# Performance work log

Measured on AMD Instinct MI355X. Metric: run time of the kernel, lower is better.

Reference implementation:

```python
import jax, jax.numpy as jnp
import numpy as np

WS = 16          # window_size
OWS = 24         # overlap_win_size = int(ws*0.5) + ws
PAD = (OWS - WS) // 2
NH = 6           # num_heads


def _ln(x, g, b):
    m = jnp.mean(x, axis=-1, keepdims=True)
    v = jnp.mean((x - m) ** 2, axis=-1, keepdims=True)
    return (x - m) * jax.lax.rsqrt(v + 1e-5) * g + b


def setup_inputs() -> dict:
    key = jax.random.key(0)
    ks = jax.random.split(key, 12)
    B, H, W, C = 4, 64, 64, 180
    std = 0.02
    x = jax.random.normal(ks[0], (B, H * W, C), jnp.float32)
    y = jax.random.normal(ks[1], (B, H * W, C), jnp.float32)
    kv_w = jax.random.normal(ks[2], (2 * C, C), jnp.float32) * std
    kv_b = jnp.zeros((2 * C,), jnp.float32)
    q_w = jax.random.normal(ks[3], (C, C), jnp.float32) * std
    q_b = jnp.zeros((C,), jnp.float32)
    rpb = jax.random.normal(ks[4], ((WS + OWS - 1) ** 2, NH), jnp.float32) * std
    proj_w = jax.random.normal(ks[5], (C, C), jnp.float32) * std
    proj_b = jnp.zeros((C,), jnp.float32)
    fc1_w = jax.random.normal(ks[6], (4 * C, C), jnp.float32) * std
    fc1_b = jnp.zeros((4 * C,), jnp.float32)
    fc2_w = jax.random.normal(ks[7], (C, 4 * C), jnp.float32) * std
    fc2_b = jnp.zeros((C,), jnp.float32)
    norm1_g = jnp.ones((C,), jnp.float32); norm1_b = jnp.zeros((C,), jnp.float32)
    norm2_g = jnp.ones((C,), jnp.float32); norm2_b = jnp.zeros((C,), jnp.float32)
    # relative position index (HAT-style OCA): query coords vs extended window coords
    co = np.stack(np.meshgrid(np.arange(WS), np.arange(WS), indexing='ij')).reshape(2, -1)   # 2, ws*ws
    ce = np.stack(np.meshgrid(np.arange(OWS), np.arange(OWS), indexing='ij')).reshape(2, -1) # 2, ows*ows
    rel = (ce[:, None, :] - co[:, :, None]).transpose(1, 2, 0) + (WS - 1)  # nq, n, 2 in [0, ws+ows-2]
    rpi = jnp.asarray(rel[..., 0] * (WS + OWS - 1) + rel[..., 1], jnp.int32)  # [256, 576]
    return {
        'x': x, 'y': y,
        'norm1_g': norm1_g, 'norm1_b': norm1_b,
        'kv_w': kv_w, 'kv_b': kv_b, 'q_w': q_w, 'q_b': q_b,
        'rpb': rpb, 'proj_w': proj_w, 'proj_b': proj_b,
        'norm2_g': norm2_g, 'norm2_b': norm2_b,
        'fc1_w': fc1_w, 'fc1_b': fc1_b, 'fc2_w': fc2_w, 'fc2_b': fc2_b,
        'rpi': rpi, 'h': 64, 'w': 64,
    }


def reference(x, y, norm1_g, norm1_b, kv_w, kv_b, q_w, q_b, rpb, proj_w, proj_b,
              norm2_g, norm2_b, fc1_w, fc1_b, fc2_w, fc2_b, rpi, h, w):
    b, L, c = x.shape
    nh = NH
    d = c // nh
    scale = d ** -0.5
    nwh, nww = h // WS, w // WS
    nq, n = WS * WS, OWS * OWS

    shortcut = x
    xn = _ln(x, norm1_g, norm1_b).reshape(b, h, w, c)
    yn = _ln(y, norm1_g, norm1_b).reshape(b, h, w, c)

    kv = xn @ kv_w.T + kv_b                                  # b,h,w,2c
    q = yn @ q_w.T + q_b                                     # b,h,w,c

    # kv -> [2, b, c, h, w] then pad spatially and extract overlapping windows (nn.Unfold)
    kv = kv.reshape(b, h, w, 2, c).transpose(3, 0, 4, 1, 2)  # 2,b,c,h,w
    kvp = jnp.pad(kv, ((0, 0), (0, 0), (0, 0), (PAD, PAD), (PAD, PAD)))
    hh = jnp.arange(nwh)[:, None] * WS + jnp.arange(OWS)[None, :]   # [nwh, OWS]
    ww = jnp.arange(nww)[:, None] * WS + jnp.arange(OWS)[None, :]   # [nww, OWS]
    patches = kvp[:, :, :, hh][:, :, :, :, :, ww]            # 2,b,c,nwh,OWS,nww,OWS
    kvw = patches.transpose(0, 1, 3, 5, 4, 6, 2).reshape(2, b * nwh * nww, n, c)
    kwin, vwin = kvw[0], kvw[1]                              # [b_, n, c]

    # non-overlapping query windows (window_partition)
    qwin = q.reshape(b, nwh, WS, nww, WS, c).transpose(0, 1, 3, 2, 4, 5).reshape(-1, nq, c)
    b_ = qwin.shape[0]

    qh = qwin.reshape(b_, nq, nh, d).transpose(0, 2, 1, 3) * scale
    kh = kwin.reshape(b_, n, nh, d).transpose(0, 2, 1, 3)
    vh = vwin.reshape(b_, n, nh, d).transpose(0, 2, 1, 3)

    attn = jnp.einsum('bhqd,bhkd->bhqk', qh, kh)             # [b_, nh, nq, n]
    bias = rpb[rpi.reshape(-1)].reshape(nq, n, nh).transpose(2, 0, 1)  # [nh, nq, n]
    attn = jax.nn.softmax(attn + bias[None], axis=-1)
    out = jnp.einsum('bhqk,bhkd->bhqd', attn, vh).transpose(0, 2, 1, 3).reshape(b_, nq, c)

    # window_reverse
    out = out.reshape(b, nwh, nww, WS, WS, c).transpose(0, 1, 3, 2, 4, 5).reshape(b, h * w, c)

    xo = out @ proj_w.T + proj_b + shortcut
    xn2 = _ln(xo, norm2_g, norm2_b)
    mlp = jax.nn.gelu(xn2 @ fc1_w.T + fc1_b, approximate=False) @ fc2_w.T + fc2_b
    return xo + mlp
```

## Files before the change

### kernel.cpp

```cpp
#include <hip/hip_runtime.h>

typedef __bf16 bf16;
typedef __bf16 bf16x8 __attribute__((ext_vector_type(8)));
typedef __bf16 bf16x4 __attribute__((ext_vector_type(4)));
typedef __bf16 bf16x2 __attribute__((ext_vector_type(2)));
typedef float f32x4 __attribute__((ext_vector_type(4)));

static __device__ __forceinline__ bf16x8 ld8(const bf16* p) {
    return *reinterpret_cast<const bf16x8*>(p);
}
static __device__ __forceinline__ bf16x4 ld4(const bf16* p) {
    return *reinterpret_cast<const bf16x4*>(p);
}
static __device__ __forceinline__ bf16x8 ld8_b32(const bf16* p) {
    bf16x8 v;
#pragma unroll
    for (int i = 0; i < 4; ++i) {
        bf16x2 t = *reinterpret_cast<const bf16x2*>(p + i * 2);
        v[i * 2] = t[0]; v[i * 2 + 1] = t[1];
    }
    return v;
}
static __device__ __forceinline__ bf16x8 zero8() {
    bf16x8 v;
#pragma unroll
    for (int i = 0; i < 8; ++i) v[i] = (bf16)0.f;
    return v;
}

#define MFMA16(a, b, c) __builtin_amdgcn_mfma_f32_16x16x32_bf16((a), (b), (c), 0, 0, 0)

template <int ROWS, int BK, int KPAD, int THREADS>
static __device__ __forceinline__ void load_chunk_g(const bf16* __restrict__ g,
                                                    bf16x8* r, int tid) {
    constexpr int TOT = ROWS * BK / 8;
    constexpr int NP = (TOT + THREADS - 1) / THREADS;
#pragma unroll
    for (int p = 0; p < NP; ++p) {
        int idx = p * THREADS + tid;
        if ((TOT % THREADS) == 0 || idx < TOT) {
            int row = idx / (BK / 8), cg = idx % (BK / 8);
            r[p] = ld8(g + (long)row * KPAD + cg * 8);
        }
    }
}
template <int ROWS, int BK, int THREADS>
static __device__ __forceinline__ void store_chunk_l(bf16* __restrict__ lds,
                                                     const bf16x8* r, int tid) {
    constexpr int TOT = ROWS * BK / 8;
    constexpr int NP = (TOT + THREADS - 1) / THREADS;
#pragma unroll
    for (int p = 0; p < NP; ++p) {
        int idx = p * THREADS + tid;
        if ((TOT % THREADS) == 0 || idx < TOT) {
            int row = idx / (BK / 8), cg = idx % (BK / 8);
            *reinterpret_cast<bf16x8*>(lds + row * 200 + cg * 8) = r[p];
        }
    }
}
template <int ROWS, int BK, int KPAD, int THREADS>
static __device__ __forceinline__ void stage_tile(const bf16* __restrict__ g,
                                                  bf16* __restrict__ lds, int tid) {
    constexpr int TOT = ROWS * BK / 8;
    constexpr int NP = (TOT + THREADS - 1) / THREADS;
#pragma unroll
    for (int p = 0; p < NP; ++p) {
        int idx = p * THREADS + tid;
        if ((TOT % THREADS) == 0 || idx < TOT) {
            int row = idx / (BK / 8), cg = idx % (BK / 8);
            bf16x8 v = ld8(g + (long)row * KPAD + cg * 8);
            *reinterpret_cast<bf16x8*>(lds + row * 200 + cg * 8) = v;
        }
    }
}

__global__ __launch_bounds__(256) void fused_pre(
    const float* __restrict__ x, const float* __restrict__ y,
    const float* __restrict__ g, const float* __restrict__ b,
    bf16* __restrict__ dst,
    const float* __restrict__ kv_w, const float* __restrict__ kv_b,
    const float* __restrict__ q_w, const float* __restrict__ q_b,
    const float* __restrict__ proj_w, const float* __restrict__ fc1_w,
    const float* __restrict__ fc2_w, const float* __restrict__ rpb,
    const int* __restrict__ rpi,
    bf16* __restrict__ wkv, bf16* __restrict__ wq, bf16* __restrict__ wproj,
    bf16* __restrict__ wfc1, bf16* __restrict__ wfc2, bf16* __restrict__ biast,
    float* __restrict__ kvbp, float* __restrict__ qbp)
{
    for (int u = blockIdx.x; u < 13635; u += 1704) {
        if (u < 8192) {
            int wave = threadIdx.x >> 6, lane = threadIdx.x & 63;
            int row = u * 4 + wave;
            const float* sp = (row < 16384) ? (x + (long)row * 180)
                                            : (y + (long)(row - 16384) * 180);
            float v0 = sp[lane];
            float v1 = sp[lane + 64];
            float v2 = (lane < 52) ? sp[lane + 128] : 0.f;
            float s = v0 + v1 + v2;
            float sq = v0 * v0 + v1 * v1 + v2 * v2;
#pragma unroll
            for (int m = 32; m >= 1; m >>= 1) {
                s += __shfl_xor(s, m);
                sq += __shfl_xor(sq, m);
            }
            float mean = s * (1.f / 180.f);
            float var = sq * (1.f / 180.f) - mean * mean;
            float rs = rsqrtf(var + 1e-5f);
            bf16* dp = dst + (long)row * 192;
            dp[lane] = (bf16)((v0 - mean) * rs * g[lane] + b[lane]);
            dp[lane + 64] = (bf16)((v1 - mean) * rs * g[lane + 64] + b[lane + 64]);
            float o2 = (lane < 52) ? ((v2 - mean) * rs * g[lane + 128] + b[lane + 128]) : 0.f;
            dp[lane + 128] = (bf16)o2;
            continue;
        }
        int i = (u - 8192) * 256 + threadIdx.x;
        if (i < 73728) {
            int n = i / 192, k = i % 192;
            int kv = n / 192, rem = n % 192, hh = rem >> 5, d = rem & 31;
            float v = (d < 30 && k < 180) ? kv_w[(kv * 180 + hh * 30 + d) * 180 + k] : 0.f;
            wkv[i] = (bf16)v;
        } else if (i < 122880) {
            int j = i - 73728; int n = j / 192, k = j % 192;
            int hh = n >> 5, d = n & 31;
            float v = (n < 192 && d < 30 && k < 180) ? q_w[(hh * 30 + d) * 180 + k] : 0.f;
            wq[j] = (bf16)v;
        } else if (i < 172032) {
            int j = i - 122880; int n = j / 192, k = j % 192;
            int hh = k >> 5, d = k & 31;
            float v = (n < 180 && d < 30) ? proj_w[n * 180 + hh * 30 + d] : 0.f;
            wproj[j] = (bf16)v;
        } else if (i < 319488) {
            int j = i - 172032; int n = j / 192, k = j % 192;
            float v = (n < 720 && k < 180) ? fc1_w[n * 180 + k] : 0.f;
            wfc1[j] = (bf16)v;
        } else if (i < 507904) {
            int j = i - 319488; int n = j / 736, k = j % 736;
            float v = (n < 180 && k < 720) ? fc2_w[n * 720 + k] : 0.f;
            wfc2[j] = (bf16)v;
        } else if (i < 1392640) {
            int t = i - 507904;
            int r = t & 3;
            int lane = (t >> 2) & 63;
            int tmp2 = t >> 8;
            int kg = tmp2 % 36;
            int tmp3 = tmp2 / 36;
            int qg = tmp3 & 15;
            int h = tmp3 >> 4;
            int q = qg * 16 + (lane & 15);
            int key = kg * 16 + ((lane >> 4) << 2) + r;
            biast[t] = (bf16)rpb[rpi[q * 576 + key] * 6 + h];
        } else if (i < 1393024) {
            int t = i - 1392640;
            int kv = t / 192, rem = t % 192, hh = rem >> 5, d = rem & 31;
            kvbp[t] = (d < 30) ? kv_b[kv * 180 + hh * 30 + d] : 0.f;
        } else if (i < 1393216) {
            int t = i - 1393024;
            int hh = t >> 5, d = t & 31;
            qbp[t] = (d < 30) ? q_b[hh * 30 + d] * 0.18257418583505537f : 0.f;
        }
    }
}

__global__ __launch_bounds__(512, 4) void gemm_kvq(
    const bf16* __restrict__ xn, const bf16* __restrict__ yn,
    const bf16* __restrict__ wkv, const bf16* __restrict__ wq,
    const float* __restrict__ kvbp, const float* __restrict__ qbp,
    bf16* __restrict__ kvbuf, bf16* __restrict__ qbuf)
{
    const int tid = threadIdx.x, wave = tid >> 6, lane = tid & 63;
    const int llo = lane & 15, quad = lane >> 4;
    const int phys = blockIdx.x;
    const int xcd = phys & 7, idx = phys >> 3;
    const int tmi = xcd * 16 + idx / 3;
    const int bz = idx % 3;
    const bool isq = (bz == 2);
    const bf16* A = isq ? yn : xn;
    const bf16* Wbase = isq ? wq : (wkv + (long)bz * 3 * 64 * 192);
    const int tm = tmi * 128;

    __shared__ __align__(16) bf16 Sa[128 * 200];
    __shared__ __align__(16) bf16 Sb[64 * 200];
    bf16* Sc = Sb;

    stage_tile<128, 192, 192, 512>(A + (long)tm * 192, Sa, tid);
    bf16x8 wreg[3];
    load_chunk_g<64, 192, 192, 512>(Wbase, wreg, tid);

    const float sc = isq ? 0.18257418583505537f : 1.f;

    for (int s = 0; s < 3; ++s) {
        if (s) __syncthreads();
        store_chunk_l<64, 192, 512>(Sb, wreg, tid);
        __syncthreads();
        if (s < 2) load_chunk_g<64, 192, 192, 512>(Wbase + (long)(s + 1) * 64 * 192, wreg, tid);

        f32x4 acc[4];
#pragma unroll
        for (int nt = 0; nt < 4; ++nt)
#pragma unroll
            for (int r = 0; r < 4; ++r) acc[nt][r] = 0.f;
#pragma unroll
        for (int kt = 0; kt < 6; ++kt) {
            bf16x8 a = ld8(Sa + (wave * 16 + llo) * 200 + kt * 32 + quad * 8);
#pragma unroll
            for (int nt = 0; nt < 4; ++nt) {
                bf16x8 b = ld8(Sb + (nt * 16 + llo) * 200 + kt * 32 + quad * 8);
                acc[nt] = MFMA16(a, b, acc[nt]);
            }
        }

        const int grp = bz * 3 + s;
        __syncthreads();
#pragma unroll
        for (int nt = 0; nt < 4; ++nt) {
            int n = grp * 64 + nt * 16 + llo;
            float bv = isq ? qbp[n - 384] : kvbp[n];
#pragma unroll
            for (int r = 0; r < 4; ++r)
                Sc[(wave * 16 + quad * 4 + r) * 72 + nt * 16 + llo] =
                    (bf16)(acc[nt][r] * sc + bv);
        }
        __syncthreads();
        const int row8 = tid >> 3, seg = tid & 7;
#pragma unroll
        for (int ps = 0; ps < 2; ++ps) {
            int row = ps * 64 + row8;
            bf16x8 vv = *reinterpret_cast<const bf16x8*>(Sc + row * 72 + seg * 8);
            long m = tm + row;
            if (!isq)
                *reinterpret_cast<bf16x8*>(kvbuf + m * 384 + grp * 64 + seg * 8) = vv;
            else
                *reinterpret_cast<bf16x8*>(qbuf + m * 192 + (grp - 6) * 64 + seg * 8) = vv;
        }
    }
}

__global__ __launch_bounds__(512, 6) void attn_kernel(
    const bf16* __restrict__ qbuf, const bf16* __restrict__ kvbuf,
    const bf16* __restrict__ biast, bf16* __restrict__ obuf)
{
    const int phys = blockIdx.x;
    const int xcd = phys & 7, idx = phys >> 3;
    const int win = xcd * 8 + idx / 12;
    const int sub = idx % 12;
    const int qhalf = sub & 1;
    const int head = sub >> 1;
    const int bb = win / 16, wi = (win % 16) / 4, wj = win % 4;
    const int tid = threadIdx.x;
    const int wave = tid >> 6, lane = tid & 63;
    const int llo = lane & 15, quad = lane >> 4;
    const int qbase = qhalf * 128 + wave * 16;
    const int qg = qhalf * 8 + wave;

    __shared__ bf16 Kc[2][64][40];
    __shared__ bf16 Vt[2][32][74];
    __shared__ bf16 Ps[8][16][72];

    const int u = tid & 255;
    const int tloc = u >> 2, dq = u & 3;
    const bool isV = tid >= 256;
    int aa = tloc / 24, w0 = tloc % 24;

    const int q0 = qbase + llo;
    const int gr_q = bb * 4096 + (wi * 16 + (q0 >> 4)) * 64 + (wj * 16 + (q0 & 15));
    const bf16x8 qf = ld8(qbuf + (long)gr_q * 192 + head * 32 + quad * 8);
    const bf16* bbase = biast + ((long)(head * 16 + qg) * 36) * 256 + lane * 4;

    {
        int gy = wi * 16 + aa - 4, gx = wj * 16 + w0 - 4;
        bf16x8 st = zero8();
        if ((unsigned)gy < 64u && (unsigned)gx < 64u) {
            long gr = (long)(bb * 4096 + gy * 64 + gx) * 384;
            st = ld8(kvbuf + gr + (isV ? 192 : 0) + head * 32 + dq * 8);
        }
        if (!isV) {
            *reinterpret_cast<bf16x8*>(&Kc[0][tloc][dq * 8]) = st;
        } else {
#pragma unroll
            for (int j = 0; j < 8; ++j) Vt[0][dq * 8 + j][tloc] = st[j];
        }
    }
    __syncthreads();

    f32x4 o[2];
    float m_run = -1e30f, l_run = 0.f;
#pragma unroll
    for (int n2 = 0; n2 < 2; ++n2)
#pragma unroll
        for (int r = 0; r < 4; ++r) o[n2][r] = 0.f;

    for (int c = 0; c < 9; ++c) {
        const int cur = c & 1;

        bf16x8 stage;
        if (c < 8) {
            w0 += 16; aa += 2;
            if (w0 >= 24) { w0 -= 24; ++aa; }
            int gy = wi * 16 + aa - 4, gx = wj * 16 + w0 - 4;
            stage = zero8();
            if ((unsigned)gy < 64u && (unsigned)gx < 64u) {
                long gr = (long)(bb * 4096 + gy * 64 + gx) * 384;
                stage = ld8(kvbuf + gr + (isV ? 192 : 0) + head * 32 + dq * 8);
            }
        }

        f32x4 s[4];
#pragma unroll
        for (int kt = 0; kt < 4; ++kt) {
            bf16x8 kf = ld8(&Kc[cur][kt * 16 + llo][quad * 8]);
            f32x4 zc;
            zc[0] = 0.f; zc[1] = 0.f; zc[2] = 0.f; zc[3] = 0.f;
            s[kt] = MFMA16(kf, qf, zc);
        }

#pragma unroll
        for (int kt = 0; kt < 4; ++kt) {
            bf16x4 bv = ld4(bbase + (c * 4 + kt) * 256);
#pragma unroll
            for (int r = 0; r < 4; ++r) s[kt][r] += (float)bv[r];
        }

        float mx = s[0][0];
#pragma unroll
        for (int kt = 0; kt < 4; ++kt)
#pragma unroll
            for (int r = 0; r < 4; ++r) mx = fmaxf(mx, s[kt][r]);
        mx = fmaxf(mx, __shfl_xor(mx, 16));
        mx = fmaxf(mx, __shfl_xor(mx, 32));
        float m_new = fmaxf(m_run, mx);
        float alpha = __expf(m_run - m_new);
        float ls = 0.f;
#pragma unroll
        for (int kt = 0; kt < 4; ++kt)
#pragma unroll
            for (int r = 0; r < 4; ++r) {
                float p = __expf(s[kt][r] - m_new);
                s[kt][r] = p;
                ls += p;
            }
        ls += __shfl_xor(ls, 16);
        ls += __shfl_xor(ls, 32);
        l_run = l_run * alpha + ls;
        m_run = m_new;

#pragma unroll
        for (int r = 0; r < 4; ++r) {
            float a = __shfl(alpha, quad * 4 + r);
            o[0][r] *= a;
            o[1][r] *= a;
        }

#pragma unroll
        for (int kt = 0; kt < 4; ++kt) {
            bf16x4 pv;
#pragma unroll
            for (int r = 0; r < 4; ++r) pv[r] = (bf16)s[kt][r];
            *reinterpret_cast<bf16x4*>(&Ps[wave][llo][kt * 16 + quad * 4]) = pv;
        }

#pragma unroll
        for (int kt2 = 0; kt2 < 2; ++kt2) {
            bf16x8 pa = ld8(&Ps[wave][llo][kt2 * 32 + quad * 8]);
#pragma unroll
            for (int n2 = 0; n2 < 2; ++n2) {
                bf16x8 vb = ld8_b32(&Vt[cur][n2 * 16 + llo][kt2 * 32 + quad * 8]);
                o[n2] = MFMA16(pa, vb, o[n2]);
            }
        }

        if (c < 8) {
            if (!isV) {
                *reinterpret_cast<bf16x8*>(&Kc[1 - cur][tloc][dq * 8]) = stage;
            } else {
#pragma unroll
                for (int j = 0; j < 8; ++j) Vt[1 - cur][dq * 8 + j][tloc] = stage[j];
            }
            __syncthreads();
        }
    }

    float linv = 1.f / l_run;
#pragma unroll
    for (int r = 0; r < 4; ++r) {
        float li = __shfl(linv, quad * 4 + r);
        int q = qbase + quad * 4 + r;
        int gr = bb * 4096 + (wi * 16 + (q >> 4)) * 64 + (wj * 16 + (q & 15));
#pragma unroll
        for (int n2 = 0; n2 < 2; ++n2)
            obuf[(long)gr * 192 + head * 32 + n2 * 16 + llo] = (bf16)(o[n2][r] * li);
    }
}

__global__ __launch_bounds__(256, 3) void gemm_projln(
    const bf16* __restrict__ obuf, const bf16* __restrict__ wproj,
    const float* __restrict__ proj_b, const float* __restrict__ x,
    const float* __restrict__ g, const float* __restrict__ bln,
    float* __restrict__ xo, bf16* __restrict__ xn2)
{
    const int tid = threadIdx.x, wave = tid >> 6, lane = tid & 63;
    const int llo = lane & 15, quad = lane >> 4;
    const int mbase = blockIdx.x * 64;

    __shared__ __align__(16) bf16 Sa[64 * 200];
    __shared__ __align__(16) bf16 Sb[64 * 200];
    stage_tile<64, 192, 192, 256>(obuf + (long)mbase * 192, Sa, tid);
    bf16x8 wreg[6];
    load_chunk_g<64, 192, 192, 256>(wproj, wreg, tid);

    f32x4 acc[12];
#pragma unroll
    for (int nt = 0; nt < 12; ++nt)
#pragma unroll
        for (int r = 0; r < 4; ++r) acc[nt][r] = 0.f;

    for (int nc = 0; nc < 3; ++nc) {
        if (nc) __syncthreads();
        store_chunk_l<64, 192, 256>(Sb, wreg, tid);
        __syncthreads();
        if (nc < 2) load_chunk_g<64, 192, 192, 256>(wproj + (long)(nc + 1) * 64 * 192, wreg, tid);
#pragma unroll
        for (int kt = 0; kt < 6; ++kt) {
            bf16x8 a = ld8(Sa + (wave * 16 + llo) * 200 + kt * 32 + quad * 8);
#pragma unroll
            for (int nt = 0; nt < 4; ++nt) {
                bf16x8 b = ld8(Sb + (nt * 16 + llo) * 200 + kt * 32 + quad * 8);
                acc[nc * 4 + nt] = MFMA16(a, b, acc[nc * 4 + nt]);
            }
        }
    }

#pragma unroll
    for (int r = 0; r < 4; ++r) {
        int m = mbase + wave * 16 + quad * 4 + r;
        float v[12];
        float sum = 0.f, sq = 0.f;
#pragma unroll
        for (int nt = 0; nt < 12; ++nt) {
            int n = nt * 16 + llo;
            float val = 0.f;
            if (n < 180) val = acc[nt][r] + proj_b[n] + x[(long)m * 180 + n];
            v[nt] = val;
            sum += val; sq += val * val;
        }
#pragma unroll
        for (int msk = 1; msk <= 8; msk <<= 1) {
            sum += __shfl_xor(sum, msk);
            sq  += __shfl_xor(sq, msk);
        }
        float mean = sum * (1.f / 180.f);
        float var = sq * (1.f / 180.f) - mean * mean;
        float rs = rsqrtf(var + 1e-5f);
#pragma unroll
        for (int nt = 0; nt < 12; ++nt) {
            int n = nt * 16 + llo;
            if (n < 180) {
                xo[(long)m * 180 + n] = v[nt];
                xn2[(long)m * 192 + n] = (bf16)((v[nt] - mean) * rs * g[n] + bln[n]);
            } else {
                xn2[(long)m * 192 + n] = (bf16)0.f;
            }
        }
    }
}

__global__ __launch_bounds__(512, 4) void gemm_fc1(
    const bf16* __restrict__ A, const bf16* __restrict__ W,
    const float* __restrict__ bias, bf16* __restrict__ outp)
{
    const int tid = threadIdx.x, wave = tid >> 6, lane = tid & 63;
    const int llo = lane & 15, quad = lane >> 4;
    const int phys = blockIdx.x;
    const int xcd = phys & 7, idx = phys >> 3;
    const int tmi = xcd * 16 + idx / 4;
    const int bz = idx % 4;
    const int tm = tmi * 128;
    const bf16* Wbase = W + (long)bz * 3 * 64 * 192;

    __shared__ __align__(16) bf16 Sa[128 * 200];
    __shared__ __align__(16) bf16 Sb[64 * 200];
    bf16* Sc = Sb;

    stage_tile<128, 192, 192, 512>(A + (long)tm * 192, Sa, tid);
    bf16x8 wreg[3];
    load_chunk_g<64, 192, 192, 512>(Wbase, wreg, tid);

    for (int s = 0; s < 3; ++s) {
        if (s) __syncthreads();
        store_chunk_l<64, 192, 512>(Sb, wreg, tid);
        __syncthreads();
        if (s < 2) load_chunk_g<64, 192, 192, 512>(Wbase + (long)(s + 1) * 64 * 192, wreg, tid);

        f32x4 acc[4];
#pragma unroll
        for (int nt = 0; nt < 4; ++nt)
#pragma unroll
            for (int r = 0; r < 4; ++r) acc[nt][r] = 0.f;
#pragma unroll
        for (int kt = 0; kt < 6; ++kt) {
            bf16x8 a = ld8(Sa + (wave * 16 + llo) * 200 + kt * 32 + quad * 8);
#pragma unroll
            for (int nt = 0; nt < 4; ++nt) {
                bf16x8 b = ld8(Sb + (nt * 16 + llo) * 200 + kt * 32 + quad * 8);
                acc[nt] = MFMA16(a, b, acc[nt]);
            }
        }

        const int nb = (bz * 3 + s) * 64;
        __syncthreads();
#pragma unroll
        for (int nt = 0; nt < 4; ++nt) {
            int n = nb + nt * 16 + llo;
            float bv = (n < 720) ? bias[n] : 0.f;
#pragma unroll
            for (int r = 0; r < 4; ++r) {
                float v = acc[nt][r] + bv;
                float gel = 0.5f * v * (1.f + erff(v * 0.7071067811865475f));
                Sc[(wave * 16 + quad * 4 + r) * 72 + nt * 16 + llo] = (bf16)gel;
            }
        }
        __syncthreads();
        const int row8 = tid >> 3, seg = tid & 7;
        if (nb + seg * 8 < 736) {
#pragma unroll
            for (int ps = 0; ps < 2; ++ps) {
                int row = ps * 64 + row8;
                bf16x8 vv = *reinterpret_cast<const bf16x8*>(Sc + row * 72 + seg * 8);
                *reinterpret_cast<bf16x8*>(outp + (long)(tm + row) * 736 + nb + seg * 8) = vv;
            }
        }
    }
}

__global__ __launch_bounds__(256, 4) void gemm_fc2(
    const bf16* __restrict__ A, const bf16* __restrict__ W,
    const float* __restrict__ bias, const float* __restrict__ resid,
    float* __restrict__ outp)
{
    const int tid = threadIdx.x, wave = tid >> 6, lane = tid & 63;
    const int llo = lane & 15, quad = lane >> 4;
    const int phys = blockIdx.x;
    const int xcd = phys & 7, idx = phys >> 3;
    const int tmi = xcd * 32 + idx / 3;
    const int tni = idx % 3;
    const int tm = tmi * 64;
    const int tn = tni * 64;

    __shared__ __align__(16) bf16 Sa[64 * 200];
    __shared__ __align__(16) bf16 Sb[64 * 200];

    const bf16* Ap = A + (long)tm * 736;
    const bf16* Wp = W + (long)tn * 736;

    bf16x8 ar[6], wr[6];
    load_chunk_g<64, 192, 736, 256>(Ap, ar, tid);
    load_chunk_g<64, 192, 736, 256>(Wp, wr, tid);

    f32x4 acc[4];
#pragma unroll
    for (int nt = 0; nt < 4; ++nt)
#pragma unroll
        for (int r = 0; r < 4; ++r) acc[nt][r] = 0.f;

#pragma unroll
    for (int c = 0; c < 4; ++c) {
        if (c) __syncthreads();
        if (c < 3) {
            store_chunk_l<64, 192, 256>(Sa, ar, tid);
            store_chunk_l<64, 192, 256>(Sb, wr, tid);
        } else {
            store_chunk_l<64, 160, 256>(Sa, ar, tid);
            store_chunk_l<64, 160, 256>(Sb, wr, tid);
        }
        __syncthreads();
        if (c < 2) {
            load_chunk_g<64, 192, 736, 256>(Ap + (c + 1) * 192, ar, tid);
            load_chunk_g<64, 192, 736, 256>(Wp + (c + 1) * 192, wr, tid);
        } else if (c == 2) {
            load_chunk_g<64, 160, 736, 256>(Ap + 576, ar, tid);
            load_chunk_g<64, 160, 736, 256>(Wp + 576, wr, tid);
        }
        const int nkt = (c == 3) ? 5 : 6;
        for (int kt = 0; kt < nkt; ++kt) {
            bf16x8 a = ld8(Sa + (wave * 16 + llo) * 200 + kt * 32 + quad * 8);
#pragma unroll
            for (int nt = 0; nt < 4; ++nt) {
                bf16x8 b = ld8(Sb + (nt * 16 + llo) * 200 + kt * 32 + quad * 8);
                acc[nt] = MFMA16(a, b, acc[nt]);
            }
        }
    }

#pragma unroll
    for (int nt = 0; nt < 4; ++nt)
#pragma unroll
        for (int r = 0; r < 4; ++r) {
            int m = tm + wave * 16 + quad * 4 + r;
            int n = tn + nt * 16 + llo;
            if (n >= 180) continue;
            float v = acc[nt][r] + bias[n];
            outp[(long)m * 180 + n] = v + resid[(long)m * 180 + n];
        }
}

extern "C" void kernel_launch(void* const* d_in, const int* in_sizes, int n_in,
                              void* d_out, int out_size, void* d_ws, size_t ws_size,
                              hipStream_t stream) {
    const float* x      = (const float*)d_in[0];
    const float* y      = (const float*)d_in[1];
    const float* n1g    = (const float*)d_in[2];
    const float* n1b    = (const float*)d_in[3];
    const float* kv_w   = (const float*)d_in[4];
    const float* kv_b   = (const float*)d_in[5];
    const float* q_w    = (const float*)d_in[6];
    const float* q_b    = (const float*)d_in[7];
    const float* rpb    = (const float*)d_in[8];
    const float* proj_w = (const float*)d_in[9];
    const float* proj_b = (const float*)d_in[10];
    const float* n2g    = (const float*)d_in[11];
    const float* n2b    = (const float*)d_in[12];
    const float* fc1_w  = (const float*)d_in[13];
    const float* fc1_b  = (const float*)d_in[14];
    const float* fc2_w  = (const float*)d_in[15];
    const float* fc2_b  = (const float*)d_in[16];
    const int*   rpi    = (const int*)d_in[17];

    char* ws = (char*)d_ws;
    bf16* xn    = (bf16*)(ws + 0);
    bf16* yn    = (bf16*)(ws + 6291456);
    bf16* qbuf  = (bf16*)(ws + 12582912);
    bf16* kvbuf = (bf16*)(ws + 18874368);
    bf16* obuf  = (bf16*)(ws + 31457280);
    float* xo   = (float*)(ws + 37748736);
    bf16* biast = (bf16*)(ws + 49545216);
    bf16* wkv   = (bf16*)(ws + 51314688);
    bf16* wq    = (bf16*)(ws + 51462144);
    bf16* wproj = (bf16*)(ws + 51560448);
    bf16* wfc1  = (bf16*)(ws + 51658752);
    bf16* wfc2  = (bf16*)(ws + 51953664);
    float* kvbp = (float*)(ws + 52428800);
    float* qbp  = (float*)(ws + 52430336);
    bf16* hmid  = (bf16*)(ws + 6291456);
    bf16* xn2   = xn;

    fused_pre<<<1704, 256, 0, stream>>>(x, y, n1g, n1b, xn,
                                        kv_w, kv_b, q_w, q_b,
                                        proj_w, fc1_w, fc2_w, rpb, rpi,
                                        wkv, wq, wproj, wfc1, wfc2, biast,
                                        kvbp, qbp);
    gemm_kvq<<<384, 512, 0, stream>>>(xn, yn, wkv, wq, kvbp, qbp, kvbuf, qbuf);
    attn_kernel<<<768, 512, 0, stream>>>(qbuf, kvbuf, biast, obuf);
    gemm_projln<<<256, 256, 0, stream>>>(obuf, wproj, proj_b, x, n2g, n2b, xo, xn2);
    gemm_fc1<<<512, 512, 0, stream>>>(xn2, wfc1, fc1_b, hmid);
    gemm_fc2<<<768, 256, 0, stream>>>(hmid, wfc2, fc2_b, xo, (float*)d_out);
}
```

Before: 195.1 us.

## Use exp2 softmax with lazy rescale, vector V loads, and MFMA priority hints

Folds log2(e) into the query scale, query bias and relative-position bias so the attention softmax can use exp2f directly. The online-softmax rescale of the running max, sum and output is skipped unless some row's max grows by more than 8 in log2 units, which cuts exp and shuffle work per chunk. The padded V tile row stride changes from 74 to 88 with 16-byte alignment so V fragments load as one 128-bit read instead of four 32-bit reads. s_setprio hints are placed around the MFMA sections. The risks are a different LDS bank-conflict pattern and slightly larger unnormalized intermediates under the lazy rescale.

```diff
diff --git a/kernel.cpp b/kernel.cpp
--- a/kernel.cpp
+++ b/kernel.cpp
@@ -6,20 +6,13 @@
 typedef __bf16 bf16x2 __attribute__((ext_vector_type(2)));
 typedef float f32x4 __attribute__((ext_vector_type(4)));
 
+#define LOG2E 1.4426950408889634f
+
 static __device__ __forceinline__ bf16x8 ld8(const bf16* p) {
     return *reinterpret_cast<const bf16x8*>(p);
 }
 static __device__ __forceinline__ bf16x4 ld4(const bf16* p) {
     return *reinterpret_cast<const bf16x4*>(p);
-}
-static __device__ __forceinline__ bf16x8 ld8_b32(const bf16* p) {
-    bf16x8 v;
-#pragma unroll
-    for (int i = 0; i < 4; ++i) {
-        bf16x2 t = *reinterpret_cast<const bf16x2*>(p + i * 2);
-        v[i * 2] = t[0]; v[i * 2 + 1] = t[1];
-    }
-    return v;
 }
 static __device__ __forceinline__ bf16x8 zero8() {
     bf16x8 v;
@@ -148,7 +141,7 @@
             int h = tmp3 >> 4;
             int q = qg * 16 + (lane & 15);
             int key = kg * 16 + ((lane >> 4) << 2) + r;
-            biast[t] = (bf16)rpb[rpi[q * 576 + key] * 6 + h];
+            biast[t] = (bf16)(rpb[rpi[q * 576 + key] * 6 + h] * LOG2E);
         } else if (i < 1393024) {
             int t = i - 1392640;
             int kv = t / 192, rem = t % 192, hh = rem >> 5, d = rem & 31;
@@ -156,7 +149,7 @@
         } else if (i < 1393216) {
             int t = i - 1393024;
             int hh = t >> 5, d = t & 31;
-            qbp[t] = (d < 30) ? q_b[hh * 30 + d] * 0.18257418583505537f : 0.f;
+            qbp[t] = (d < 30) ? q_b[hh * 30 + d] * (0.18257418583505537f * LOG2E) : 0.f;
         }
     }
 }
@@ -186,7 +179,7 @@
     bf16x8 wreg[3];
     load_chunk_g<64, 192, 192, 512>(Wbase, wreg, tid);
 
-    const float sc = isq ? 0.18257418583505537f : 1.f;
+    const float sc = isq ? (0.18257418583505537f * LOG2E) : 1.f;
 
     for (int s = 0; s < 3; ++s) {
         if (s) __syncthreads();
@@ -253,7 +246,7 @@
     const int qg = qhalf * 8 + wave;
 
     __shared__ bf16 Kc[2][64][40];
-    __shared__ bf16 Vt[2][32][74];
+    __shared__ __align__(16) bf16 Vt[2][32][88];
     __shared__ bf16 Ps[8][16][72];
 
     const int u = tid & 255;
@@ -305,6 +298,7 @@
         }
 
         f32x4 s[4];
+        __builtin_amdgcn_s_setprio(1);
 #pragma unroll
         for (int kt = 0; kt < 4; ++kt) {
             bf16x8 kf = ld8(&Kc[cur][kt * 16 + llo][quad * 8]);
@@ -312,6 +306,7 @@
             zc[0] = 0.f; zc[1] = 0.f; zc[2] = 0.f; zc[3] = 0.f;
             s[kt] = MFMA16(kf, qf, zc);
         }
+        __builtin_amdgcn_s_setprio(0);
 
 #pragma unroll
         for (int kt = 0; kt < 4; ++kt) {
@@ -327,28 +322,32 @@
             for (int r = 0; r < 4; ++r) mx = fmaxf(mx, s[kt][r]);
         mx = fmaxf(mx, __shfl_xor(mx, 16));
         mx = fmaxf(mx, __shfl_xor(mx, 32));
-        float m_new = fmaxf(m_run, mx);
-        float alpha = __expf(m_run - m_new);
+
+        if (!__all(mx - m_run <= 8.f)) {
+            float m_new = fmaxf(m_run, mx);
+            float alpha = exp2f(m_run - m_new);
+            l_run *= alpha;
+#pragma unroll
+            for (int r = 0; r < 4; ++r) {
+                float a = __shfl(alpha, quad * 4 + r);
+                o[0][r] *= a;
+                o[1][r] *= a;
+            }
+            m_run = m_new;
+        }
+
         float ls = 0.f;
 #pragma unroll
         for (int kt = 0; kt < 4; ++kt)
 #pragma unroll
             for (int r = 0; r < 4; ++r) {
-                float p = __expf(s[kt][r] - m_new);
+                float p = exp2f(s[kt][r] - m_run);
                 s[kt][r] = p;
                 ls += p;
             }
         ls += __shfl_xor(ls, 16);
         ls += __shfl_xor(ls, 32);
-        l_run = l_run * alpha + ls;
-        m_run = m_new;
-
-#pragma unroll
-        for (int r = 0; r < 4; ++r) {
-            float a = __shfl(alpha, quad * 4 + r);
-            o[0][r] *= a;
-            o[1][r] *= a;
-        }
+        l_run += ls;
 
 #pragma unroll
         for (int kt = 0; kt < 4; ++kt) {
@@ -358,15 +357,17 @@
             *reinterpret_cast<bf16x4*>(&Ps[wave][llo][kt * 16 + quad * 4]) = pv;
         }
 
+        __builtin_amdgcn_s_setprio(1);
 #pragma unroll
         for (int kt2 = 0; kt2 < 2; ++kt2) {
             bf16x8 pa = ld8(&Ps[wave][llo][kt2 * 32 + quad * 8]);
 #pragma unroll
             for (int n2 = 0; n2 < 2; ++n2) {
-                bf16x8 vb = ld8_b32(&Vt[cur][n2 * 16 + llo][kt2 * 32 + quad * 8]);
+                bf16x8 vb = ld8(&Vt[cur][n2 * 16 + llo][kt2 * 32 + quad * 8]);
                 o[n2] = MFMA16(pa, vb, o[n2]);
             }
         }
+        __builtin_amdgcn_s_setprio(0);
 
         if (c < 8) {
             if (!isV) {
```

New measurement: 197.4 us. No clear change (+1.2%).
